# Kernel optimization log

Measured on AMD Instinct MI355X. Metric: run time of the kernel, lower is better.

Reference implementation:

```python
import jax, jax.numpy as jnp
import numpy as np

D_MODEL, N_HEADS, D_K = 768, 12, 64
LN_EPS = 1e-5


def setup_inputs() -> dict:
    key = jax.random.key(0)
    ks = jax.random.split(key, 8)
    b, c, n, s = 8, 32, 4, 64
    scale = 1.0 / np.sqrt(D_MODEL)
    inp = {
        "e": jax.random.normal(ks[0], (b, c, n, s, D_MODEL), dtype=jnp.float32),
        "h": jax.random.normal(ks[1], (b, c, s, D_MODEL), dtype=jnp.float32),
        # weights stored [in, out] (torch Linear transposed)
        "Wq": jax.random.normal(ks[2], (D_MODEL, N_HEADS * D_K), dtype=jnp.float32) * scale,
        "bq": jnp.zeros((N_HEADS * D_K,), dtype=jnp.float32),
        "Wk": jax.random.normal(ks[3], (D_MODEL, N_HEADS * D_K), dtype=jnp.float32) * scale,
        "bk": jnp.zeros((N_HEADS * D_K,), dtype=jnp.float32),
        "Wv": jax.random.normal(ks[4], (D_MODEL, N_HEADS * D_K), dtype=jnp.float32) * scale,
        "bv": jnp.zeros((N_HEADS * D_K,), dtype=jnp.float32),
        "Wo": jax.random.normal(ks[5], (N_HEADS * D_K, D_MODEL), dtype=jnp.float32) * scale,
        "bo": jnp.zeros((D_MODEL,), dtype=jnp.float32),
        "ln_g": jnp.ones((D_MODEL,), dtype=jnp.float32),
        "ln_b": jnp.zeros((D_MODEL,), dtype=jnp.float32),
    }
    return inp


def _layer_norm(x, g, b):
    mu = jnp.mean(x, axis=-1, keepdims=True)
    var = jnp.mean(jnp.square(x - mu), axis=-1, keepdims=True)
    return (x - mu) * jax.lax.rsqrt(var + LN_EPS) * g + b


def reference(e, h, Wq, bq, Wk, bk, Wv, bv, Wo, bo, ln_g, ln_b):
    # e: [b, c, n, i, d]  h: [b, c, j, d]
    e_res = e
    en = _layer_norm(e, ln_g, ln_b)
    b, c, n, i, _ = e.shape
    j = h.shape[2]
    q = (en @ Wq + bq).reshape(b, c, n, i, N_HEADS, D_K)
    k = (h @ Wk + bk).reshape(b, c, j, N_HEADS, D_K)
    v = (h @ Wv + bv).reshape(b, c, j, N_HEADS, D_K)
    attn = jnp.einsum('bcnihd,bcjhd->bcnhij', q, k) * (1.0 / np.sqrt(D_K))
    attn = jax.nn.softmax(attn, axis=-1)
    o = jnp.einsum('bcnhij,bcjhd->bcnihd', attn, v).reshape(b, c, n, i, N_HEADS * D_K)
    return o @ Wo + bo + e_res
```

## Files before the change

kernel.cpp:

```cpp
#include <hip/hip_runtime.h>

typedef __bf16 bf16x8 __attribute__((ext_vector_type(8)));
typedef __bf16 bf16x4 __attribute__((ext_vector_type(4)));
typedef float f32x4 __attribute__((ext_vector_type(4)));

__device__ __forceinline__ f32x4 mfma16(bf16x8 a, bf16x8 b, f32x4 c) {
  return __builtin_amdgcn_mfma_f32_16x16x32_bf16(a, b, c, 0, 0, 0);
}

template <int NWG>
__device__ __forceinline__ int xcd_swz(int orig) {
  constexpr int NX = 8;
  constexpr int q = NWG / NX;
  constexpr int r = NWG % NX;
  const int xcd = orig % NX;
  const int pos = orig / NX;
  if constexpr (r == 0) {
    return xcd * q + pos;
  } else {
    return (xcd < r ? xcd * (q + 1) : r * (q + 1) + (xcd - r) * q) + pos;
  }
}

__global__ __launch_bounds__(256) void prep_w_kernel(
    const float* __restrict__ Wq, const float* __restrict__ Wk,
    const float* __restrict__ Wv, const float* __restrict__ Wo,
    __bf16* __restrict__ WqT, __bf16* __restrict__ WkvT, __bf16* __restrict__ WoT) {
  __shared__ float tile[32][33];
  const int z = blockIdx.z;
  const float* W = (z == 0) ? Wq : (z == 1) ? Wk : (z == 2) ? Wv : Wo;
  __bf16* out = (z == 0) ? WqT : (z == 3) ? WoT : WkvT;
  const int rowOff = (z == 2) ? 768 : 0;
  const int tx = threadIdx.x, ty = threadIdx.y;
  const int x = blockIdx.x * 32 + tx;
  const int y = blockIdx.y * 32 + ty;
#pragma unroll
  for (int i = 0; i < 32; i += 8) tile[ty + i][tx] = W[(size_t)(y + i) * 768 + x];
  __syncthreads();
  const int nx = blockIdx.y * 32 + tx;
  const int ny = blockIdx.x * 32 + ty;
#pragma unroll
  for (int i = 0; i < 32; i += 8)
    out[(size_t)(rowOff + ny + i) * 768 + nx] = (__bf16)tile[tx][ty + i];
}

__global__ __launch_bounds__(256) void ln_stats_kernel(
    const float* __restrict__ e, float* __restrict__ mu, float* __restrict__ rs) {
  const int lane = threadIdx.x & 63;
  const int wid = threadIdx.x >> 6;
  const size_t row = (size_t)blockIdx.x * 4 + wid;
  const float* p = e + row * 768;
  float x[12];
  float sum = 0.f;
#pragma unroll
  for (int s = 0; s < 3; ++s) {
    f32x4 v = *(const f32x4*)(p + (s * 64 + lane) * 4);
#pragma unroll
    for (int q = 0; q < 4; ++q) { x[s * 4 + q] = v[q]; sum += v[q]; }
  }
#pragma unroll
  for (int d = 1; d < 64; d <<= 1) sum += __shfl_xor(sum, d);
  const float m = sum * (1.f / 768.f);
  float vs = 0.f;
#pragma unroll
  for (int q = 0; q < 12; ++q) { float d = x[q] - m; vs += d * d; }
#pragma unroll
  for (int d = 1; d < 64; d <<= 1) vs += __shfl_xor(vs, d);
  if (lane == 0) { mu[row] = m; rs[row] = rsqrtf(vs * (1.f / 768.f) + 1e-5f); }
}

enum { MODE_Q = 0, MODE_KV = 1, MODE_O = 2 };

template <int MODE, int NC, int NWG>
__global__ __launch_bounds__(256) void gemm_kernel(
    const float* __restrict__ Afp,
    const __bf16* __restrict__ Abf,
    const __bf16* __restrict__ WT,
    const float* __restrict__ bias0, const float* __restrict__ bias1,
    const float* __restrict__ mu, const float* __restrict__ rs,
    const float* __restrict__ gamma, const float* __restrict__ beta,
    __bf16* __restrict__ dst0, __bf16* __restrict__ dst1,
    float* __restrict__ outp) {
  __shared__ __bf16 As[128][72];
  __shared__ __bf16 Bs[128][72];
  const int wgid = xcd_swz<NWG>(blockIdx.x);
  const int rowBase = (wgid / NC) * 128;
  const int colBase = (wgid % NC) * 128;
  const int t = threadIdx.x;
  const int lane = t & 63, wid = t >> 6;
  const int wm = wid >> 1, wn = wid & 1;
  const int lr = lane & 15, lg = lane >> 4;
  f32x4 acc[4][4] = {};
  for (int kb = 0; kb < 12; ++kb) {
#pragma unroll
    for (int s = 0; s < 8; ++s) {
      const int li = (s * 256 + t) * 4;
      const int row = li >> 6, kcol = li & 63;
      const int r = rowBase + row;
      bf16x4 pk;
      if constexpr (MODE == MODE_O) {
        pk = *(const bf16x4*)(Abf + ((((size_t)(r >> 6)) * 12 + kb) << 12) + ((r & 63) << 6) + kcol);
      } else {
        f32x4 v = *(const f32x4*)(Afp + (size_t)r * 768 + kb * 64 + kcol);
        if constexpr (MODE == MODE_Q) {
          const float m = mu[r], rr = rs[r];
          f32x4 g4 = *(const f32x4*)(gamma + kb * 64 + kcol);
          f32x4 b4 = *(const f32x4*)(beta + kb * 64 + kcol);
#pragma unroll
          for (int q = 0; q < 4; ++q) v[q] = (v[q] - m) * rr * g4[q] + b4[q];
        }
#pragma unroll
        for (int q = 0; q < 4; ++q) pk[q] = (__bf16)v[q];
      }
      *(bf16x4*)&As[row][kcol] = pk;
    }
#pragma unroll
    for (int s = 0; s < 8; ++s) {
      const int li = (s * 256 + t) * 4;
      const int n = li >> 6, k = li & 63;
      *(bf16x4*)&Bs[n][k] = *(const bf16x4*)(WT + (size_t)(colBase + n) * 768 + kb * 64 + k);
    }
    __syncthreads();
#pragma unroll
    for (int kc = 0; kc < 2; ++kc) {
      bf16x8 a[4], b[4];
#pragma unroll
      for (int it = 0; it < 4; ++it)
        a[it] = *(const bf16x8*)&As[wm * 64 + it * 16 + lr][kc * 32 + lg * 8];
#pragma unroll
      for (int jt = 0; jt < 4; ++jt)
        b[jt] = *(const bf16x8*)&Bs[wn * 64 + jt * 16 + lr][kc * 32 + lg * 8];
#pragma unroll
      for (int it = 0; it < 4; ++it)
#pragma unroll
        for (int jt = 0; jt < 4; ++jt)
          acc[it][jt] = mfma16(a[it], b[jt], acc[it][jt]);
    }
    __syncthreads();
  }
  const int roww = rowBase + wm * 64;
  const int colw = colBase + wn * 64;
#pragma unroll
  for (int it = 0; it < 4; ++it) {
#pragma unroll
    for (int jt = 0; jt < 4; ++jt) {
      const int c = colw + jt * 16 + lr;
#pragma unroll
      for (int rg = 0; rg < 4; ++rg) {
        const int r = roww + it * 16 + lg * 4 + rg;
        const float val = acc[it][jt][rg];
        if constexpr (MODE == MODE_O) {
          outp[(size_t)r * 768 + c] = val + bias0[c] + Afp[(size_t)r * 768 + c];
        } else if constexpr (MODE == MODE_Q) {
          dst0[((((size_t)(r >> 6)) * 12 + (c >> 6)) << 12) + ((r & 63) << 6) + (c & 63)] =
              (__bf16)(val + bias0[c]);
        } else {
          if (c < 768) {
            dst0[((((size_t)(r >> 6)) * 12 + (c >> 6)) << 12) + ((r & 63) << 6) + (c & 63)] =
                (__bf16)(val + bias0[c]);
          } else {
            const int c2 = c - 768;
            dst1[((((size_t)(r >> 6)) * 12 + (c2 >> 6)) << 12) + ((c2 & 63) << 6) + (r & 63)] =
                (__bf16)(val + bias1[c2]);
          }
        }
      }
    }
  }
}

__global__ __launch_bounds__(64) void attn_kernel(
    const __bf16* __restrict__ q, const __bf16* __restrict__ k,
    const __bf16* __restrict__ v, __bf16* __restrict__ o) {
  const int gid = xcd_swz<12288>(blockIdx.x);
  const int n = gid & 3;
  const int bh = gid >> 2;
  const int h = bh % 12;
  const int bc = bh / 12;
  const __bf16* qp = q + (((size_t)(bc * 4 + n) * 12 + h) << 12);
  const __bf16* kp = k + (((size_t)bc * 12 + h) << 12);
  const __bf16* vp = v + (((size_t)bc * 12 + h) << 12);
  __bf16* op = o + (((size_t)(bc * 4 + n) * 12 + h) << 12);
  const int lane = threadIdx.x;
  const int lr = lane & 15, lg = lane >> 4;
  __shared__ __bf16 P[64][72];

  bf16x8 qf[4][2], kf[4][2];
#pragma unroll
  for (int it = 0; it < 4; ++it)
#pragma unroll
    for (int kc = 0; kc < 2; ++kc)
      qf[it][kc] = *(const bf16x8*)(qp + (it * 16 + lr) * 64 + kc * 32 + lg * 8);
#pragma unroll
  for (int jt = 0; jt < 4; ++jt)
#pragma unroll
    for (int kc = 0; kc < 2; ++kc)
      kf[jt][kc] = *(const bf16x8*)(kp + (jt * 16 + lr) * 64 + kc * 32 + lg * 8);

  f32x4 s[4][4] = {};
#pragma unroll
  for (int kc = 0; kc < 2; ++kc)
#pragma unroll
    for (int jt = 0; jt < 4; ++jt)
#pragma unroll
      for (int it = 0; it < 4; ++it)
        s[jt][it] = mfma16(kf[jt][kc], qf[it][kc], s[jt][it]);

  float recip[4];
#pragma unroll
  for (int it = 0; it < 4; ++it) {
    float m = -1e30f;
#pragma unroll
    for (int jt = 0; jt < 4; ++jt)
#pragma unroll
      for (int rg = 0; rg < 4; ++rg) m = fmaxf(m, s[jt][it][rg]);
    m = fmaxf(m, __shfl_xor(m, 16));
    m = fmaxf(m, __shfl_xor(m, 32));
    float sum = 0.f;
#pragma unroll
    for (int jt = 0; jt < 4; ++jt) {
      bf16x4 pk;
#pragma unroll
      for (int rg = 0; rg < 4; ++rg) {
        float p = __expf((s[jt][it][rg] - m) * 0.125f);
        sum += p;
        pk[rg] = (__bf16)p;
      }
      *(bf16x4*)&P[it * 16 + lr][jt * 16 + lg * 4] = pk;
    }
    sum += __shfl_xor(sum, 16);
    sum += __shfl_xor(sum, 32);
    recip[it] = 1.f / sum;
  }
  __syncthreads();

  bf16x8 vf[4][2];
#pragma unroll
  for (int dt = 0; dt < 4; ++dt)
#pragma unroll
    for (int kc = 0; kc < 2; ++kc)
      vf[dt][kc] = *(const bf16x8*)(vp + (dt * 16 + lr) * 64 + kc * 32 + lg * 8);
  f32x4 oacc[4][4] = {};
#pragma unroll
  for (int kc = 0; kc < 2; ++kc) {
    bf16x8 pf[4];
#pragma unroll
    for (int it = 0; it < 4; ++it)
      pf[it] = *(const bf16x8*)&P[it * 16 + lr][kc * 32 + lg * 8];
#pragma unroll
    for (int dt = 0; dt < 4; ++dt)
#pragma unroll
      for (int it = 0; it < 4; ++it)
        oacc[dt][it] = mfma16(vf[dt][kc], pf[it], oacc[dt][it]);
  }
#pragma unroll
  for (int it = 0; it < 4; ++it) {
    const float rc = recip[it];
#pragma unroll
    for (int dt = 0; dt < 4; ++dt) {
      bf16x4 pk;
#pragma unroll
      for (int rg = 0; rg < 4; ++rg) pk[rg] = (__bf16)(oacc[dt][it][rg] * rc);
      *(bf16x4*)(op + (size_t)(it * 16 + lr) * 64 + dt * 16 + lg * 4) = pk;
    }
  }
}

extern "C" void kernel_launch(void* const* d_in, const int* in_sizes, int n_in,
                              void* d_out, int out_size, void* d_ws, size_t ws_size,
                              hipStream_t stream) {
  const float* e  = (const float*)d_in[0];
  const float* h  = (const float*)d_in[1];
  const float* Wq = (const float*)d_in[2];
  const float* bq = (const float*)d_in[3];
  const float* Wk = (const float*)d_in[4];
  const float* bk = (const float*)d_in[5];
  const float* Wv = (const float*)d_in[6];
  const float* bv = (const float*)d_in[7];
  const float* Wo = (const float*)d_in[8];
  const float* bo = (const float*)d_in[9];
  const float* g  = (const float*)d_in[10];
  const float* b  = (const float*)d_in[11];
  float* outp = (float*)d_out;
  char* ws = (char*)d_ws;

  __bf16* WqT  = (__bf16*)(ws);
  __bf16* WkvT = (__bf16*)(ws + 1179648);
  __bf16* WoT  = (__bf16*)(ws + 3538944);
  float*  muP  = (float*)(ws + 4718592);
  float*  rsP  = (float*)(ws + 4980736);
  __bf16* k_ws = (__bf16*)(ws + 5242880);
  __bf16* v_ws = (__bf16*)(ws + 30408704);
  __bf16* q_ws = (__bf16*)(ws + 55574528);

  prep_w_kernel<<<dim3(24, 24, 4), dim3(32, 8), 0, stream>>>(Wq, Wk, Wv, Wo, WqT, WkvT, WoT);
  ln_stats_kernel<<<16384, 256, 0, stream>>>(e, muP, rsP);
  gemm_kernel<MODE_Q, 6, 3072><<<3072, 256, 0, stream>>>(
      e, nullptr, WqT, bq, nullptr, muP, rsP, g, b, q_ws, nullptr, nullptr);
  gemm_kernel<MODE_KV, 12, 1536><<<1536, 256, 0, stream>>>(
      h, nullptr, WkvT, bk, bv, nullptr, nullptr, nullptr, nullptr, k_ws, v_ws, nullptr);
  attn_kernel<<<12288, 64, 0, stream>>>(q_ws, k_ws, v_ws, q_ws);
  gemm_kernel<MODE_O, 6, 3072><<<3072, 256, 0, stream>>>(
      e, q_ws, WoT, bo, nullptr, nullptr, nullptr, nullptr, nullptr, nullptr, nullptr, outp);
}
```

Baseline: 539.2 us.

## Pre-normalize and cast GEMM inputs to bf16 and stage tiles with direct global-to-LDS loads

LayerNorm now writes a normalized bf16 copy of e, and a new cast kernel converts h to bf16, so every GEMM reads bf16 A operands. The GEMM tile loads switch to global_load_lds 16-byte direct-to-LDS transfers with an unpadded 64-wide layout, replacing register staging and the per-element normalize/convert work. This adds extra full passes that write and reread the en and h_bf buffers. The unpadded LDS rows may also cause bank conflicts on the MFMA fragment reads.

```diff
diff --git a/kernel.cpp b/kernel.cpp
--- a/kernel.cpp
+++ b/kernel.cpp
@@ -6,6 +6,12 @@
 
 __device__ __forceinline__ f32x4 mfma16(bf16x8 a, bf16x8 b, f32x4 c) {
   return __builtin_amdgcn_mfma_f32_16x16x32_bf16(a, b, c, 0, 0, 0);
+}
+
+__device__ __forceinline__ void load_lds16(const void* g, void* l) {
+  __builtin_amdgcn_global_load_lds(
+      (const __attribute__((address_space(1))) void*)g,
+      (__attribute__((address_space(3))) void*)l, 16, 0, 0);
 }
 
 template <int NWG>
@@ -44,8 +50,9 @@
     out[(size_t)(rowOff + ny + i) * 768 + nx] = (__bf16)tile[tx][ty + i];
 }
 
-__global__ __launch_bounds__(256) void ln_stats_kernel(
-    const float* __restrict__ e, float* __restrict__ mu, float* __restrict__ rs) {
+__global__ __launch_bounds__(256) void ln_kernel(
+    const float* __restrict__ e, const float* __restrict__ gam,
+    const float* __restrict__ bet, __bf16* __restrict__ en) {
   const int lane = threadIdx.x & 63;
   const int wid = threadIdx.x >> 6;
   const size_t row = (size_t)blockIdx.x * 4 + wid;
@@ -66,23 +73,44 @@
   for (int q = 0; q < 12; ++q) { float d = x[q] - m; vs += d * d; }
 #pragma unroll
   for (int d = 1; d < 64; d <<= 1) vs += __shfl_xor(vs, d);
-  if (lane == 0) { mu[row] = m; rs[row] = rsqrtf(vs * (1.f / 768.f) + 1e-5f); }
+  const float rr = rsqrtf(vs * (1.f / 768.f) + 1e-5f);
+  __bf16* o = en + row * 768;
+#pragma unroll
+  for (int s = 0; s < 3; ++s) {
+    f32x4 g4 = *(const f32x4*)(gam + (s * 64 + lane) * 4);
+    f32x4 b4 = *(const f32x4*)(bet + (s * 64 + lane) * 4);
+    bf16x4 pk;
+#pragma unroll
+    for (int q = 0; q < 4; ++q) pk[q] = (__bf16)((x[s * 4 + q] - m) * rr * g4[q] + b4[q]);
+    *(bf16x4*)(o + (s * 64 + lane) * 4) = pk;
+  }
+}
+
+__global__ __launch_bounds__(256) void cast_kernel(
+    const float* __restrict__ in, __bf16* __restrict__ out, int n4) {
+  int i = blockIdx.x * 256 + threadIdx.x;
+  const int stride = gridDim.x * 256;
+  for (; i < n4; i += stride) {
+    f32x4 v = ((const f32x4*)in)[i];
+    bf16x4 o;
+#pragma unroll
+    for (int q = 0; q < 4; ++q) o[q] = (__bf16)v[q];
+    ((bf16x4*)out)[i] = o;
+  }
 }
 
 enum { MODE_Q = 0, MODE_KV = 1, MODE_O = 2 };
 
 template <int MODE, int NC, int NWG>
 __global__ __launch_bounds__(256) void gemm_kernel(
-    const float* __restrict__ Afp,
-    const __bf16* __restrict__ Abf,
+    const __bf16* __restrict__ A,
     const __bf16* __restrict__ WT,
     const float* __restrict__ bias0, const float* __restrict__ bias1,
-    const float* __restrict__ mu, const float* __restrict__ rs,
-    const float* __restrict__ gamma, const float* __restrict__ beta,
+    const float* __restrict__ eres,
     __bf16* __restrict__ dst0, __bf16* __restrict__ dst1,
     float* __restrict__ outp) {
-  __shared__ __bf16 As[128][72];
-  __shared__ __bf16 Bs[128][72];
+  __shared__ __bf16 As[8192];
+  __shared__ __bf16 Bs[8192];
   const int wgid = xcd_swz<NWG>(blockIdx.x);
   const int rowBase = (wgid / NC) * 128;
   const int colBase = (wgid % NC) * 128;
@@ -90,35 +118,24 @@
   const int lane = t & 63, wid = t >> 6;
   const int wm = wid >> 1, wn = wid & 1;
   const int lr = lane & 15, lg = lane >> 4;
+  const int srow = lane >> 3;
+  const int skcol = (lane & 7) * 8;
   f32x4 acc[4][4] = {};
   for (int kb = 0; kb < 12; ++kb) {
 #pragma unroll
-    for (int s = 0; s < 8; ++s) {
-      const int li = (s * 256 + t) * 4;
-      const int row = li >> 6, kcol = li & 63;
-      const int r = rowBase + row;
-      bf16x4 pk;
+    for (int s = 0; s < 4; ++s) {
+      const int chunk = s * 4 + wid;
+      const int rowIn = chunk * 8 + srow;
+      const __bf16* ga;
       if constexpr (MODE == MODE_O) {
-        pk = *(const bf16x4*)(Abf + ((((size_t)(r >> 6)) * 12 + kb) << 12) + ((r & 63) << 6) + kcol);
+        const int r = rowBase + rowIn;
+        ga = A + ((((size_t)(r >> 6)) * 12 + kb) << 12) + ((r & 63) << 6) + skcol;
       } else {
-        f32x4 v = *(const f32x4*)(Afp + (size_t)r * 768 + kb * 64 + kcol);
-        if constexpr (MODE == MODE_Q) {
-          const float m = mu[r], rr = rs[r];
-          f32x4 g4 = *(const f32x4*)(gamma + kb * 64 + kcol);
-          f32x4 b4 = *(const f32x4*)(beta + kb * 64 + kcol);
-#pragma unroll
-          for (int q = 0; q < 4; ++q) v[q] = (v[q] - m) * rr * g4[q] + b4[q];
-        }
-#pragma unroll
-        for (int q = 0; q < 4; ++q) pk[q] = (__bf16)v[q];
+        ga = A + (size_t)(rowBase + rowIn) * 768 + kb * 64 + skcol;
       }
-      *(bf16x4*)&As[row][kcol] = pk;
-    }
-#pragma unroll
-    for (int s = 0; s < 8; ++s) {
-      const int li = (s * 256 + t) * 4;
-      const int n = li >> 6, k = li & 63;
-      *(bf16x4*)&Bs[n][k] = *(const bf16x4*)(WT + (size_t)(colBase + n) * 768 + kb * 64 + k);
+      load_lds16(ga, &As[chunk * 512]);
+      const __bf16* gb = WT + (size_t)(colBase + rowIn) * 768 + kb * 64 + skcol;
+      load_lds16(gb, &Bs[chunk * 512]);
     }
     __syncthreads();
 #pragma unroll
@@ -126,10 +143,10 @@
       bf16x8 a[4], b[4];
 #pragma unroll
       for (int it = 0; it < 4; ++it)
-        a[it] = *(const bf16x8*)&As[wm * 64 + it * 16 + lr][kc * 32 + lg * 8];
+        a[it] = *(const bf16x8*)&As[(wm * 64 + it * 16 + lr) * 64 + kc * 32 + lg * 8];
 #pragma unroll
       for (int jt = 0; jt < 4; ++jt)
-        b[jt] = *(const bf16x8*)&Bs[wn * 64 + jt * 16 + lr][kc * 32 + lg * 8];
+        b[jt] = *(const bf16x8*)&Bs[(wn * 64 + jt * 16 + lr) * 64 + kc * 32 + lg * 8];
 #pragma unroll
       for (int it = 0; it < 4; ++it)
 #pragma unroll
@@ -150,7 +167,7 @@
         const int r = roww + it * 16 + lg * 4 + rg;
         const float val = acc[it][jt][rg];
         if constexpr (MODE == MODE_O) {
-          outp[(size_t)r * 768 + c] = val + bias0[c] + Afp[(size_t)r * 768 + c];
+          outp[(size_t)r * 768 + c] = val + bias0[c] + eres[(size_t)r * 768 + c];
         } else if constexpr (MODE == MODE_Q) {
           dst0[((((size_t)(r >> 6)) * 12 + (c >> 6)) << 12) + ((r & 63) << 6) + (c & 63)] =
               (__bf16)(val + bias0[c]);
@@ -287,19 +304,21 @@
   __bf16* WqT  = (__bf16*)(ws);
   __bf16* WkvT = (__bf16*)(ws + 1179648);
   __bf16* WoT  = (__bf16*)(ws + 3538944);
-  float*  muP  = (float*)(ws + 4718592);
-  float*  rsP  = (float*)(ws + 4980736);
-  __bf16* k_ws = (__bf16*)(ws + 5242880);
-  __bf16* v_ws = (__bf16*)(ws + 30408704);
-  __bf16* q_ws = (__bf16*)(ws + 55574528);
+  char* R1 = ws + 4718592;
+  __bf16* en    = (__bf16*)(R1);
+  __bf16* h_bf  = (__bf16*)(R1);
+  __bf16* k_ws  = (__bf16*)(R1 + 25165824);
+  __bf16* v_ws  = (__bf16*)(R1 + 50331648);
+  __bf16* q_ws  = (__bf16*)(ws + 105381888);
 
   prep_w_kernel<<<dim3(24, 24, 4), dim3(32, 8), 0, stream>>>(Wq, Wk, Wv, Wo, WqT, WkvT, WoT);
-  ln_stats_kernel<<<16384, 256, 0, stream>>>(e, muP, rsP);
+  ln_kernel<<<16384, 256, 0, stream>>>(e, g, b, en);
   gemm_kernel<MODE_Q, 6, 3072><<<3072, 256, 0, stream>>>(
-      e, nullptr, WqT, bq, nullptr, muP, rsP, g, b, q_ws, nullptr, nullptr);
+      en, WqT, bq, nullptr, nullptr, q_ws, nullptr, nullptr);
+  cast_kernel<<<2048, 256, 0, stream>>>(h, h_bf, 16384 * 768 / 4);
   gemm_kernel<MODE_KV, 12, 1536><<<1536, 256, 0, stream>>>(
-      h, nullptr, WkvT, bk, bv, nullptr, nullptr, nullptr, nullptr, k_ws, v_ws, nullptr);
+      h_bf, WkvT, bk, bv, nullptr, k_ws, v_ws, nullptr);
   attn_kernel<<<12288, 64, 0, stream>>>(q_ws, k_ws, v_ws, q_ws);
   gemm_kernel<MODE_O, 6, 3072><<<3072, 256, 0, stream>>>(
-      e, q_ws, WoT, bo, nullptr, nullptr, nullptr, nullptr, nullptr, nullptr, nullptr, outp);
-}
+      q_ws, WoT, bo, nullptr, e, nullptr, nullptr, outp);
+}
```

Result: slower. 552.0 us (+2.4%).
